# Kernel tuning notes

Measured on AMD Instinct MI355X. Metric: run time of the kernel, lower is better.

The kernel has to match this reference:

```python
import jax, jax.numpy as jnp
import numpy as np

B, T, TAU = 4, 512, 512
D_MODEL = 1024  # in_dim == out_dim (required: pos embedding dim out_dim feeds pos_proj with in_size=in_dim)
H, D = 16, 64
LN_EPS = 1e-5


def rel_shift(x):
    # x: [B, T, L, H] -> Transformer-XL relative shift
    b, t, l, h = x.shape
    x = jnp.pad(x, ((0, 0), (0, 0), (1, 0), (0, 0)))  # pad j-dim front
    x = x.reshape(b, l + 1, t, h)[:, 1:, :, :]
    return x.reshape(b, t, l, h)


def setup_inputs() -> dict:
    key = jax.random.key(0)
    ks = jax.random.split(key, 7)
    s = 0.02
    return {
        "inputs": jax.random.normal(ks[0], (B, T, D_MODEL), jnp.float32),
        "memory": jax.random.normal(ks[1], (B, TAU, D_MODEL), jnp.float32),
        "w_qkv": jax.random.normal(ks[2], (3 * H * D, D_MODEL), jnp.float32) * s,
        "w_pos": jax.random.normal(ks[3], (H * D, D_MODEL), jnp.float32) * s,
        "w_out": jax.random.normal(ks[4], (D_MODEL, H * D), jnp.float32) * s,
        "uvar": jax.random.normal(ks[5], (H, D), jnp.float32) * s,
        "vvar": jax.random.normal(ks[6], (H, D), jnp.float32) * s,
        "ln_gamma": jnp.ones((D_MODEL,), jnp.float32),
        "ln_beta": jnp.zeros((D_MODEL,), jnp.float32),
    }


def reference(inputs, memory, w_qkv, w_pos, w_out, uvar, vvar, ln_gamma, ln_beta):
    b, t, din = inputs.shape
    tau = memory.shape[1]
    L = tau + t
    h, d = uvar.shape

    x = jnp.concatenate([jax.lax.stop_gradient(memory), inputs], axis=1)  # [B,L,Din]
    # input layernorm
    mu = jnp.mean(x, axis=-1, keepdims=True)
    var = jnp.mean((x - mu) ** 2, axis=-1, keepdims=True)
    x = (x - mu) / jnp.sqrt(var + LN_EPS) * ln_gamma + ln_beta

    qkv = x @ w_qkv.T  # [B,L,3HD]
    q, k, v = jnp.split(qkv, 3, axis=-1)
    q = q[:, -t:].reshape(b, t, h, d)
    k = k.reshape(b, L, h, d)
    v = v.reshape(b, L, h, d)

    # sinusoidal relative position embedding, dim = out_dim (= din here)
    inv_freq = 1.0 / (10000.0 ** (jnp.arange(0, din, 2, dtype=jnp.float32) / din))
    pos = jnp.arange(L - 1, -1, -1, dtype=jnp.float32)
    sin_in = pos[:, None] * inv_freq[None, :]                 # [L, din/2]
    phi = jnp.concatenate([jnp.sin(sin_in), jnp.cos(sin_in)], axis=-1)  # [L, din]
    R = (phi @ w_pos.T).reshape(L, h, d)

    score = jnp.einsum('bihd,bjhd->bijh', q + uvar, k)        # content score
    pos_score = jnp.einsum('bihd,jhd->bijh', q + vvar, R)     # position score
    score = (score + rel_shift(pos_score)) / (d ** 0.5)       # [B,T,L,H]

    # causal mask: query i attends to j <= tau + i
    mask = (jnp.arange(L)[None, :] <= (tau + jnp.arange(t))[:, None]).astype(score.dtype)
    mask = mask[None, :, :, None]
    masked = score * mask + 1e30 * (mask - 1.0)
    w = jax.nn.softmax(masked, axis=2)

    out = jnp.einsum('bijh,bjhd->bihd', w, v).reshape(b, t, h * d)
    return out @ w_out.T
```

## Files before the change

### kernel.cpp

```cpp
#include <hip/hip_runtime.h>
#include <math.h>

#define B_   4
#define T_   512
#define TAU_ 512
#define L_   1024
#define DM_  1024
#define H_   16
#define D_   64

typedef short  s16x8 __attribute__((ext_vector_type(8)));
typedef ushort u16x4 __attribute__((ext_vector_type(4)));
typedef float  f32x4 __attribute__((ext_vector_type(4)));

__device__ __forceinline__ ushort f2bf(float x) {
  uint u = __float_as_uint(x);
  u += 0x7fffu + ((u >> 16) & 1u);
  return (ushort)(u >> 16);
}
__device__ __forceinline__ float bf2f(ushort u) {
  return __uint_as_float(((uint)u) << 16);
}
__device__ __forceinline__ int sw64(int row, int col) {
  return row * 64 + (col ^ ((row & 7) << 3));
}

__global__ __launch_bounds__(256) void prep_kernel(
    const float* __restrict__ inp, const float* __restrict__ mem,
    const float* __restrict__ gamma, const float* __restrict__ beta,
    ushort* __restrict__ xn, ushort* __restrict__ phi,
    const float* __restrict__ wq, ushort* __restrict__ wqb,
    const float* __restrict__ wp, ushort* __restrict__ wpb,
    const float* __restrict__ wo, ushort* __restrict__ wob) {
  int blk = blockIdx.x;
  int t = threadIdx.x;
  if (blk < 1024) {
    int wid = t >> 6, lane = t & 63;
    int row = blk * 4 + wid;
    int b = row >> 10, l = row & 1023;
    const float* src = (l < TAU_)
        ? mem + ((size_t)b * TAU_ + l) * DM_
        : inp + ((size_t)b * T_ + (l - TAU_)) * DM_;
    float4 v[4];
    float s1 = 0.f, s2 = 0.f;
#pragma unroll
    for (int c = 0; c < 4; ++c) {
      v[c] = *(const float4*)(src + c * 256 + lane * 4);
      s1 += v[c].x + v[c].y + v[c].z + v[c].w;
      s2 += v[c].x * v[c].x + v[c].y * v[c].y + v[c].z * v[c].z + v[c].w * v[c].w;
    }
#pragma unroll
    for (int off = 32; off > 0; off >>= 1) {
      s1 += __shfl_xor(s1, off);
      s2 += __shfl_xor(s2, off);
    }
    float mu   = s1 * (1.0f / DM_);
    float var  = s2 * (1.0f / DM_) - mu * mu;
    float rstd = 1.0f / sqrtf(var + 1e-5f);
#pragma unroll
    for (int c = 0; c < 4; ++c) {
      float4 g  = *(const float4*)(gamma + c * 256 + lane * 4);
      float4 be = *(const float4*)(beta  + c * 256 + lane * 4);
      u16x4 o;
      o[0] = f2bf((v[c].x - mu) * rstd * g.x + be.x);
      o[1] = f2bf((v[c].y - mu) * rstd * g.y + be.y);
      o[2] = f2bf((v[c].z - mu) * rstd * g.z + be.z);
      o[3] = f2bf((v[c].w - mu) * rstd * g.w + be.w);
      *(u16x4*)(xn + (size_t)row * DM_ + c * 256 + lane * 4) = o;
    }
  } else if (blk < 2048) {
    int base = (blk - 1024) * 1024 + t;
#pragma unroll
    for (int it = 0; it < 4; ++it) {
      int idx = base + it * 256;
      int m = idx >> 10, c = idx & 1023;
      float p = (float)(1023 - m);
      int cc = (c < 512) ? c : c - 512;
      float invf = __expf(-((float)(2 * cc) * (1.0f / 1024.0f)) * 9.210340371976184f);
      float a = p * invf;
      phi[idx] = f2bf((c < 512) ? __sinf(a) : __cosf(a));
    }
  } else {
    int base = (blk - 2048) * 1024 + t;
#pragma unroll
    for (int it = 0; it < 4; ++it) {
      int i = base + it * 256;
      const float* src; ushort* dst; int off;
      if (i < 786432)       { src = wq; dst = wqb; off = i; }
      else if (i < 1048576) { src = wp; dst = wpb; off = i - 786432; }
      else                  { src = wo; dst = wob; off = i - 1048576; }
      float4 v = *(const float4*)(src + (size_t)off * 4);
      u16x4 o = { f2bf(v.x), f2bf(v.y), f2bf(v.z), f2bf(v.w) };
      *(u16x4*)(dst + (size_t)off * 4) = o;
    }
  }
}

template <typename CT>
__device__ __forceinline__ void gemm_nt_body_n64(
    const ushort* __restrict__ Arows, const ushort* __restrict__ Brows,
    CT* __restrict__ Crows, int ldc, int K) {
  __shared__ __attribute__((aligned(16))) ushort As[128 * 64];
  __shared__ __attribute__((aligned(16))) ushort Bs[64 * 64];
  int t = threadIdx.x;
  int w = t >> 6, lane = t & 63, g = lane >> 4, low = lane & 15;
  int wr = w >> 1, wc = w & 1;
  f32x4 acc[4][2] = {};

  for (int kt = 0; kt < K; kt += 64) {
    __syncthreads();
#pragma unroll
    for (int q = 0; q < 4; ++q) {
      int c = t + q * 256;
      int row = c >> 3;
      int gslot = (c & 7) ^ (row & 7);
      const ushort* ga = Arows + (size_t)row * K + kt + gslot * 8;
      __builtin_amdgcn_global_load_lds(
          (const __attribute__((address_space(1))) void*)ga,
          (__attribute__((address_space(3))) void*)&As[(q * 256 + w * 64) * 8],
          16, 0, 0);
    }
#pragma unroll
    for (int q = 0; q < 2; ++q) {
      int c = t + q * 256;
      int row = c >> 3;
      int gslot = (c & 7) ^ (row & 7);
      const ushort* gb = Brows + (size_t)row * K + kt + gslot * 8;
      __builtin_amdgcn_global_load_lds(
          (const __attribute__((address_space(1))) void*)gb,
          (__attribute__((address_space(3))) void*)&Bs[(q * 256 + w * 64) * 8],
          16, 0, 0);
    }
    __syncthreads();

#pragma unroll
    for (int kc = 0; kc < 2; ++kc) {
      s16x8 af[4], bfr[2];
#pragma unroll
      for (int mi = 0; mi < 4; ++mi) {
        int row = wr * 64 + mi * 16 + low;
        af[mi] = *(const s16x8*)&As[row * 64 + (((4 * kc + g) ^ (row & 7)) * 8)];
      }
#pragma unroll
      for (int ni = 0; ni < 2; ++ni) {
        int col = wc * 32 + ni * 16 + low;
        bfr[ni] = *(const s16x8*)&Bs[col * 64 + (((4 * kc + g) ^ (col & 7)) * 8)];
      }
#pragma unroll
      for (int mi = 0; mi < 4; ++mi)
#pragma unroll
        for (int ni = 0; ni < 2; ++ni)
          acc[mi][ni] = __builtin_amdgcn_mfma_f32_16x16x32_bf16(
              af[mi], bfr[ni], acc[mi][ni], 0, 0, 0);
    }
  }
#pragma unroll
  for (int mi = 0; mi < 4; ++mi)
#pragma unroll
    for (int ni = 0; ni < 2; ++ni)
#pragma unroll
      for (int r = 0; r < 4; ++r) {
        int m = wr * 64 + mi * 16 + 4 * g + r;
        int n = wc * 32 + ni * 16 + low;
        if constexpr (sizeof(CT) == 2)
          Crows[(size_t)m * ldc + n] = f2bf(acc[mi][ni][r]);
        else
          Crows[(size_t)m * ldc + n] = acc[mi][ni][r];
      }
}

__global__ __launch_bounds__(256) void qkv_r_gemm(
    const ushort* __restrict__ xnb, const ushort* __restrict__ wqb,
    ushort* __restrict__ qkvB,
    const ushort* __restrict__ phib, const ushort* __restrict__ wpb,
    ushort* __restrict__ RmB) {
  int orig = blockIdx.x;
  int id = (orig & 7) * 176 + (orig >> 3);
  if (id < 1024) {
    int by = id >> 5, bx = id & 31;
    gemm_nt_body_n64<ushort>(
        xnb + (size_t)by * 128 * 1024,
        wqb + (size_t)(1024 + bx * 64) * 1024,
        qkvB + (size_t)by * 128 * 3072 + 1024 + bx * 64, 3072, 1024);
  } else if (id < 1280) {
    int q = id - 1024;
    int by = q >> 4, bx = q & 15;
    int b = by >> 2;
    size_t arow = (size_t)b * 1024 + 512 + (by & 3) * 128;
    gemm_nt_body_n64<ushort>(
        xnb + arow * 1024,
        wqb + (size_t)bx * 64 * 1024,
        qkvB + arow * 3072 + bx * 64, 3072, 1024);
  } else {
    int rr = id - 1280;
    int by = rr >> 4, bx = rr & 15;
    gemm_nt_body_n64<ushort>(
        phib + (size_t)by * 128 * 1024,
        wpb + (size_t)bx * 64 * 1024,
        RmB + (size_t)by * 128 * 1024 + bx * 64, 1024, 1024);
  }
}

__global__ __launch_bounds__(256) void out_gemm(
    const ushort* __restrict__ attnb, const ushort* __restrict__ wob,
    float* __restrict__ out) {
  int orig = blockIdx.x;
  int id = (orig & 7) * 32 + (orig >> 3);
  int by = id >> 4, bx = id & 15;
  gemm_nt_body_n64<float>(
      attnb + (size_t)by * 128 * 1024,
      wob + (size_t)bx * 64 * 1024,
      out + (size_t)by * 128 * 1024 + bx * 64, 1024, 1024);
}

__global__ __launch_bounds__(256) void attn_mfma_kernel(
    const ushort* __restrict__ qkv, const ushort* __restrict__ Rm,
    const float* __restrict__ uvar, const float* __restrict__ vvar,
    ushort* __restrict__ attn) {
  __shared__ __attribute__((aligned(16))) ushort Ks[2][64 * 64];
  __shared__ __attribute__((aligned(16))) ushort Vt[2][64 * 64];
  __shared__ __attribute__((aligned(16))) ushort Rs[2][128 * 64];
  __shared__ __attribute__((aligned(16))) ushort Pp[4][16 * 64];

  int t   = threadIdx.x;
  int w   = t >> 6;
  int lw  = t & 63;
  int g   = lw >> 4;
  int low = lw & 15;

  int orig = blockIdx.x;
  int bid  = (orig & 7) * 64 + (orig >> 3);
  int s    = bid & 7;
  int h    = (bid >> 3) & 15;
  int b    = bid >> 7;
  int bi   = (s & 1) ? (7 - (s >> 1)) : (s >> 1);
  int i0   = bi * 64;
  int lb_w = 48 - 16 * w;

  auto stage_kr = [&](int buf, int tl) {
    int j0s = tl * 64;
#pragma unroll
    for (int q = 0; q < 2; ++q) {
      int c = t + q * 256;
      int row = c >> 3;
      int sl = (c & 7) ^ (row & 7);
      const ushort* srck = qkv + (size_t)(b * L_ + j0s + row) * 3072 +
                           1024 + h * 64 + sl * 8;
      __builtin_amdgcn_global_load_lds(
          (const __attribute__((address_space(1))) void*)srck,
          (__attribute__((address_space(3))) void*)&Ks[buf][(q * 256 + w * 64) * 8],
          16, 0, 0);
    }
    int mb = j0s + 448 - i0;
#pragma unroll
    for (int q = 0; q < 4; ++q) {
      int c = t + q * 256;
      int row = c >> 3;
      int m = mb + row; m = (m > 1023) ? 1023 : m;
      int sl = (c & 7) ^ (row & 7);
      const ushort* srcr = Rm + (size_t)m * 1024 + h * 64 + sl * 8;
      __builtin_amdgcn_global_load_lds(
          (const __attribute__((address_space(1))) void*)srcr,
          (__attribute__((address_space(3))) void*)&Rs[buf][(q * 256 + w * 64) * 8],
          16, 0, 0);
    }
  };

  int vj  = t & 63;
  int vd0 = (t >> 6) * 8;
  float4 vreg[2];
  auto vload = [&](int tl) {
    const ushort* p = qkv + (size_t)(b * L_ + tl * 64 + vj) * 3072 + 2048 + h * 64;
    vreg[0] = *(const float4*)(p + vd0);
    vreg[1] = *(const float4*)(p + vd0 + 32);
  };
  auto vwrite = [&](int buf) {
#pragma unroll
    for (int it = 0; it < 2; ++it) {
      ushort vals[8];
      *(float4*)vals = vreg[it];
#pragma unroll
      for (int e = 0; e < 8; ++e) {
        int d = it * 32 + vd0 + e;
        Vt[buf][d * 64 + (vj ^ ((d & 7) << 3))] = vals[e];
      }
    }
  };

  int iq = i0 + 16 * w + low;
  s16x8 qu[2], qv[2];
  {
    const ushort* qrow = qkv + (size_t)(b * L_ + TAU_ + iq) * 3072 + h * 64;
    const float* ur = uvar + h * 64;
    const float* vr = vvar + h * 64;
#pragma unroll
    for (int kc = 0; kc < 2; ++kc) {
      int dbase = kc * 32 + 8 * g;
#pragma unroll
      for (int e = 0; e < 8; ++e) {
        float q = bf2f(qrow[dbase + e]);
        qu[kc][e] = (short)f2bf(q + ur[dbase + e]);
        qv[kc][e] = (short)f2bf(q + vr[dbase + e]);
      }
    }
  }

  f32x4 O[4] = {};
  float mreg[4] = {-INFINITY, -INFINITY, -INFINITY, -INFINITY};
  float lreg[4] = {0.f, 0.f, 0.f, 0.f};

  int ntiles = 9 + bi;
  stage_kr(0, 0);
  vload(0);
  vwrite(0);
  __syncthreads();
  int cur = 0;
  for (int tile = 0; tile < ntiles; ++tile) {
    int j0 = tile * 64;
    bool more = (tile + 1 < ntiles);
    if (more) { stage_kr(cur ^ 1, tile + 1); vload(tile + 1); }

    f32x4 s4[4] = {};
#pragma unroll
    for (int jt = 0; jt < 4; ++jt) {
#pragma unroll
      for (int kc = 0; kc < 2; ++kc) {
        s16x8 kb = *(const s16x8*)&Ks[cur][sw64(jt * 16 + low, kc * 32 + 8 * g)];
        s4[jt] = __builtin_amdgcn_mfma_f32_16x16x32_bf16(qu[kc], kb, s4[jt], 0, 0, 0);
      }
    }
    f32x4 p[5] = {};
#pragma unroll
    for (int mt = 0; mt < 5; ++mt) {
#pragma unroll
      for (int kc = 0; kc < 2; ++kc) {
        s16x8 rb = *(const s16x8*)&Rs[cur][sw64(lb_w + mt * 16 + low, kc * 32 + 8 * g)];
        p[mt] = __builtin_amdgcn_mfma_f32_16x16x32_bf16(qv[kc], rb, p[mt], 0, 0, 0);
      }
    }
#pragma unroll
    for (int r = 0; r < 4; ++r) {
      int iL = 4 * g + r;
      int src = g * 16 + ((low + 15 - iL) & 15);
      float sh0 = __shfl(p[0][r], src);
      float sh1 = __shfl(p[1][r], src);
      float sh2 = __shfl(p[2][r], src);
      float sh3 = __shfl(p[3][r], src);
      float sh4 = __shfl(p[4][r], src);
      bool lo = (low <= iL);
      float po0 = lo ? sh0 : sh1;
      float po1 = lo ? sh1 : sh2;
      float po2 = lo ? sh2 : sh3;
      float po3 = lo ? sh3 : sh4;
      int lim = TAU_ + i0 + 16 * w + iL;
      s4[0][r] = (j0 +  0 + low <= lim) ? (s4[0][r] + po0) * 0.125f : -1e30f;
      s4[1][r] = (j0 + 16 + low <= lim) ? (s4[1][r] + po1) * 0.125f : -1e30f;
      s4[2][r] = (j0 + 32 + low <= lim) ? (s4[2][r] + po2) * 0.125f : -1e30f;
      s4[3][r] = (j0 + 48 + low <= lim) ? (s4[3][r] + po3) * 0.125f : -1e30f;
    }
#pragma unroll
    for (int r = 0; r < 4; ++r) {
      float mx = fmaxf(fmaxf(s4[0][r], s4[1][r]), fmaxf(s4[2][r], s4[3][r]));
      mx = fmaxf(mx, __shfl_xor(mx, 1));
      mx = fmaxf(mx, __shfl_xor(mx, 2));
      mx = fmaxf(mx, __shfl_xor(mx, 4));
      mx = fmaxf(mx, __shfl_xor(mx, 8));
      float mn = fmaxf(mreg[r], mx);
      float alpha = __expf(mreg[r] - mn);
      mreg[r] = mn;
      float sum = 0.f;
#pragma unroll
      for (int jt = 0; jt < 4; ++jt) {
        float pe = __expf(s4[jt][r] - mn);
        s4[jt][r] = pe;
        sum += pe;
      }
      sum += __shfl_xor(sum, 1);
      sum += __shfl_xor(sum, 2);
      sum += __shfl_xor(sum, 4);
      sum += __shfl_xor(sum, 8);
      lreg[r] = lreg[r] * alpha + sum;
      O[0][r] *= alpha; O[1][r] *= alpha; O[2][r] *= alpha; O[3][r] *= alpha;
    }
#pragma unroll
    for (int jt = 0; jt < 4; ++jt)
#pragma unroll
      for (int r = 0; r < 4; ++r)
        Pp[w][sw64(4 * g + r, jt * 16 + low)] = f2bf(s4[jt][r]);
    asm volatile("s_waitcnt lgkmcnt(0)" ::: "memory");
    s16x8 pa0 = *(const s16x8*)&Pp[w][sw64(low, 8 * g)];
    s16x8 pa1 = *(const s16x8*)&Pp[w][sw64(low, 32 + 8 * g)];
#pragma unroll
    for (int dt = 0; dt < 4; ++dt) {
      s16x8 v0 = *(const s16x8*)&Vt[cur][sw64(dt * 16 + low, 8 * g)];
      s16x8 v1 = *(const s16x8*)&Vt[cur][sw64(dt * 16 + low, 32 + 8 * g)];
      O[dt] = __builtin_amdgcn_mfma_f32_16x16x32_bf16(pa0, v0, O[dt], 0, 0, 0);
      O[dt] = __builtin_amdgcn_mfma_f32_16x16x32_bf16(pa1, v1, O[dt], 0, 0, 0);
    }
    if (more) vwrite(cur ^ 1);
    __syncthreads();
    cur ^= 1;
  }
  float inv[4];
#pragma unroll
  for (int r = 0; r < 4; ++r) inv[r] = 1.0f / lreg[r];
#pragma unroll
  for (int dt = 0; dt < 4; ++dt)
#pragma unroll
    for (int r = 0; r < 4; ++r)
      attn[((size_t)(b * T_ + i0 + 16 * w + 4 * g + r)) * 1024 +
           h * 64 + dt * 16 + low] = f2bf(O[dt][r] * inv[r]);
}

extern "C" void kernel_launch(void* const* d_in, const int* in_sizes, int n_in,
                              void* d_out, int out_size, void* d_ws, size_t ws_size,
                              hipStream_t stream) {
  const float* inputs = (const float*)d_in[0];
  const float* memory = (const float*)d_in[1];
  const float* w_qkv  = (const float*)d_in[2];
  const float* w_pos  = (const float*)d_in[3];
  const float* w_out  = (const float*)d_in[4];
  const float* uvar   = (const float*)d_in[5];
  const float* vvar   = (const float*)d_in[6];
  const float* gamma  = (const float*)d_in[7];
  const float* beta   = (const float*)d_in[8];
  float* out = (float*)d_out;

  ushort* qkvB = (ushort*)d_ws;
  ushort* xnb  = qkvB + (size_t)4096 * 3072;
  ushort* phib = xnb  + (size_t)4096 * 1024;
  ushort* RmB  = phib + (size_t)1024 * 1024;
  ushort* wqb  = RmB  + (size_t)1024 * 1024;
  ushort* wpb  = wqb  + (size_t)3072 * 1024;
  ushort* wob  = wpb  + (size_t)1024 * 1024;
  ushort* attnb = xnb;

  prep_kernel<<<3328, 256, 0, stream>>>(inputs, memory, gamma, beta, xnb,
                                        phib, w_qkv, wqb, w_pos, wpb, w_out, wob);
  qkv_r_gemm<<<1408, 256, 0, stream>>>(xnb, wqb, qkvB, phib, wpb, RmB);
  attn_mfma_kernel<<<dim3(B_ * H_ * 8), 256, 0, stream>>>(qkvB, RmB, uvar, vvar, attnb);
  out_gemm<<<256, 256, 0, stream>>>(attnb, wob, out);
}
```

Measured before the change: 190.8 us.

## Split attention KV range across two blocks and merge partial softmax results

The attention kernel now splits each query tile's key range into two halves, one per block, doubling the grid to 1024 blocks. Each block writes unnormalized fp32 partial outputs plus its running max and sum, and a new merge kernel combines the two halves and writes the bf16 attention output. The R position tiles are also read straight from global memory into registers instead of being staged in LDS, which cuts LDS use and lifts the launch bound. The aim is more parallelism and better load balance, paid for with an extra launch, fp32 partial traffic, and uncoalesced global loads of R.

```diff
diff --git a/kernel.cpp b/kernel.cpp
--- a/kernel.cpp
+++ b/kernel.cpp
@@ -213,13 +213,12 @@
       out + (size_t)by * 128 * 1024 + bx * 64, 1024, 1024);
 }
 
-__global__ __launch_bounds__(256) void attn_mfma_kernel(
+__global__ void attn_mfma_kernel(
     const ushort* __restrict__ qkv, const ushort* __restrict__ Rm,
     const float* __restrict__ uvar, const float* __restrict__ vvar,
-    ushort* __restrict__ attn) {
+    float* __restrict__ Opart, float* __restrict__ Mp, float* __restrict__ Lp) {
   __shared__ __attribute__((aligned(16))) ushort Ks[2][64 * 64];
   __shared__ __attribute__((aligned(16))) ushort Vt[2][64 * 64];
-  __shared__ __attribute__((aligned(16))) ushort Rs[2][128 * 64];
   __shared__ __attribute__((aligned(16))) ushort Pp[4][16 * 64];
 
   int t   = threadIdx.x;
@@ -229,15 +228,18 @@
   int low = lw & 15;
 
   int orig = blockIdx.x;
-  int bid  = (orig & 7) * 64 + (orig >> 3);
-  int s    = bid & 7;
-  int h    = (bid >> 3) & 15;
-  int b    = bid >> 7;
-  int bi   = (s & 1) ? (7 - (s >> 1)) : (s >> 1);
+  int lin  = (orig & 7) * 128 + (orig >> 3);
+  int fam  = lin >> 4;
+  int s    = lin & 15;
+  int slot = s >> 1;
+  int half = s & 1;
+  int h    = fam & 15;
+  int b    = fam >> 4;
+  int bi   = (slot & 1) ? (7 - (slot >> 1)) : (slot >> 1);
   int i0   = bi * 64;
   int lb_w = 48 - 16 * w;
 
-  auto stage_kr = [&](int buf, int tl) {
+  auto stage_k = [&](int buf, int tl) {
     int j0s = tl * 64;
 #pragma unroll
     for (int q = 0; q < 2; ++q) {
@@ -251,19 +253,6 @@
           (__attribute__((address_space(3))) void*)&Ks[buf][(q * 256 + w * 64) * 8],
           16, 0, 0);
     }
-    int mb = j0s + 448 - i0;
-#pragma unroll
-    for (int q = 0; q < 4; ++q) {
-      int c = t + q * 256;
-      int row = c >> 3;
-      int m = mb + row; m = (m > 1023) ? 1023 : m;
-      int sl = (c & 7) ^ (row & 7);
-      const ushort* srcr = Rm + (size_t)m * 1024 + h * 64 + sl * 8;
-      __builtin_amdgcn_global_load_lds(
-          (const __attribute__((address_space(1))) void*)srcr,
-          (__attribute__((address_space(3))) void*)&Rs[buf][(q * 256 + w * 64) * 8],
-          16, 0, 0);
-    }
   };
 
   int vj  = t & 63;
@@ -309,17 +298,29 @@
   float mreg[4] = {-INFINITY, -INFINITY, -INFINITY, -INFINITY};
   float lreg[4] = {0.f, 0.f, 0.f, 0.f};
 
-  int ntiles = 9 + bi;
-  stage_kr(0, 0);
-  vload(0);
+  int nt_tot = 9 + bi;
+  int nt0    = (nt_tot + 1) >> 1;
+  int tstart = half ? nt0 : 0;
+  int tend   = half ? nt_tot : nt0;
+
+  stage_k(0, tstart);
+  vload(tstart);
   vwrite(0);
   __syncthreads();
   int cur = 0;
-  for (int tile = 0; tile < ntiles; ++tile) {
+  for (int tile = tstart; tile < tend; ++tile) {
     int j0 = tile * 64;
-    bool more = (tile + 1 < ntiles);
-    if (more) { stage_kr(cur ^ 1, tile + 1); vload(tile + 1); }
-
+    bool more = (tile + 1 < tend);
+    if (more) { stage_k(cur ^ 1, tile + 1); vload(tile + 1); }
+
+    int mb = j0 + 448 - i0;
+    s16x8 rb[5];
+#pragma unroll
+    for (int mt = 0; mt < 5; ++mt) {
+      int m = mb + lb_w + mt * 16 + low;
+      m = (m > 1023) ? 1023 : m;
+      rb[mt] = *(const s16x8*)(Rm + (size_t)m * 1024 + h * 64 + 8 * g);
+    }
     f32x4 s4[4] = {};
 #pragma unroll
     for (int jt = 0; jt < 4; ++jt) {
@@ -331,13 +332,18 @@
     }
     f32x4 p[5] = {};
 #pragma unroll
+    for (int mt = 0; mt < 5; ++mt)
+      p[mt] = __builtin_amdgcn_mfma_f32_16x16x32_bf16(qv[0], rb[mt], p[mt], 0, 0, 0);
+#pragma unroll
     for (int mt = 0; mt < 5; ++mt) {
-#pragma unroll
-      for (int kc = 0; kc < 2; ++kc) {
-        s16x8 rb = *(const s16x8*)&Rs[cur][sw64(lb_w + mt * 16 + low, kc * 32 + 8 * g)];
-        p[mt] = __builtin_amdgcn_mfma_f32_16x16x32_bf16(qv[kc], rb, p[mt], 0, 0, 0);
-      }
-    }
+      int m = mb + lb_w + mt * 16 + low;
+      m = (m > 1023) ? 1023 : m;
+      rb[mt] = *(const s16x8*)(Rm + (size_t)m * 1024 + h * 64 + 32 + 8 * g);
+    }
+#pragma unroll
+    for (int mt = 0; mt < 5; ++mt)
+      p[mt] = __builtin_amdgcn_mfma_f32_16x16x32_bf16(qv[1], rb[mt], p[mt], 0, 0, 0);
+
 #pragma unroll
     for (int r = 0; r < 4; ++r) {
       int iL = 4 * g + r;
@@ -401,15 +407,51 @@
     __syncthreads();
     cur ^= 1;
   }
-  float inv[4];
-#pragma unroll
-  for (int r = 0; r < 4; ++r) inv[r] = 1.0f / lreg[r];
+  size_t pbase = (size_t)lin * 4096;
 #pragma unroll
   for (int dt = 0; dt < 4; ++dt)
 #pragma unroll
     for (int r = 0; r < 4; ++r)
-      attn[((size_t)(b * T_ + i0 + 16 * w + 4 * g + r)) * 1024 +
-           h * 64 + dt * 16 + low] = f2bf(O[dt][r] * inv[r]);
+      Opart[pbase + (size_t)(16 * w + 4 * g + r) * 64 + dt * 16 + low] = O[dt][r];
+  if (low == 0) {
+#pragma unroll
+    for (int r = 0; r < 4; ++r) {
+      Mp[lin * 64 + 16 * w + 4 * g + r] = mreg[r];
+      Lp[lin * 64 + 16 * w + 4 * g + r] = lreg[r];
+    }
+  }
+}
+
+__global__ __launch_bounds__(256) void attn_merge_kernel(
+    const float* __restrict__ Opart, const float* __restrict__ Mp,
+    const float* __restrict__ Lp, ushort* __restrict__ attn) {
+  int id = blockIdx.x;
+  int fam = id >> 3, slot = id & 7;
+  int bi = (slot & 1) ? (7 - (slot >> 1)) : (slot >> 1);
+  int b = fam >> 4, h = fam & 15;
+  int i0 = bi * 64;
+  int t = threadIdx.x;
+  int row = t >> 2;
+  int c0  = (t & 3) * 16;
+  int p0i = id * 2, p1i = id * 2 + 1;
+  float m0 = Mp[p0i * 64 + row], m1 = Mp[p1i * 64 + row];
+  float l0 = Lp[p0i * 64 + row], l1 = Lp[p1i * 64 + row];
+  float m  = fmaxf(m0, m1);
+  float a0 = __expf(m0 - m), a1 = __expf(m1 - m);
+  float inv = 1.0f / (l0 * a0 + l1 * a1);
+  const float4* O0 = (const float4*)(Opart + (size_t)p0i * 4096 + row * 64 + c0);
+  const float4* O1 = (const float4*)(Opart + (size_t)p1i * 4096 + row * 64 + c0);
+  ushort* dst = attn + ((size_t)(b * T_ + i0 + row)) * 1024 + h * 64 + c0;
+#pragma unroll
+  for (int q = 0; q < 4; ++q) {
+    float4 x0 = O0[q], x1 = O1[q];
+    u16x4 o;
+    o[0] = f2bf((x0.x * a0 + x1.x * a1) * inv);
+    o[1] = f2bf((x0.y * a0 + x1.y * a1) * inv);
+    o[2] = f2bf((x0.z * a0 + x1.z * a1) * inv);
+    o[3] = f2bf((x0.w * a0 + x1.w * a1) * inv);
+    *(u16x4*)(dst + q * 4) = o;
+  }
 }
 
 extern "C" void kernel_launch(void* const* d_in, const int* in_sizes, int n_in,
@@ -433,11 +475,15 @@
   ushort* wqb  = RmB  + (size_t)1024 * 1024;
   ushort* wpb  = wqb  + (size_t)3072 * 1024;
   ushort* wob  = wpb  + (size_t)1024 * 1024;
+  float*  Opart = (float*)(wob + (size_t)1024 * 1024);
+  float*  Mp    = Opart + (size_t)1024 * 4096;
+  float*  Lp    = Mp + 1024 * 64;
   ushort* attnb = xnb;
 
   prep_kernel<<<3328, 256, 0, stream>>>(inputs, memory, gamma, beta, xnb,
                                         phib, w_qkv, wqb, w_pos, wpb, w_out, wob);
   qkv_r_gemm<<<1408, 256, 0, stream>>>(xnb, wqb, qkvB, phib, wpb, RmB);
-  attn_mfma_kernel<<<dim3(B_ * H_ * 8), 256, 0, stream>>>(qkvB, RmB, uvar, vvar, attnb);
+  attn_mfma_kernel<<<1024, 256, 0, stream>>>(qkvB, RmB, uvar, vvar, Opart, Mp, Lp);
+  attn_merge_kernel<<<512, 256, 0, stream>>>(Opart, Mp, Lp, attnb);
   out_gemm<<<256, 256, 0, stream>>>(attnb, wob, out);
 }
```

After: 244.6 us. 28.2% more time.
